# Kernel tuning notes

Measured on AMD Instinct MI355X. Metric: run time of the kernel, lower is better.

The kernel has to match this reference:

```python
import math
import jax, jax.numpy as jnp
import numpy as np

D_MODEL = 1024
H_HEADS = 16
D_K = D_MODEL // H_HEADS


def setup_inputs() -> dict:
    key = jax.random.key(0)
    ks = jax.random.split(key, 7)
    B, L = 4, 2048
    q = jax.random.normal(ks[0], (B, L, D_MODEL), dtype=jnp.float32)
    k = jax.random.normal(ks[1], (B, L, D_MODEL), dtype=jnp.float32)
    v = jax.random.normal(ks[2], (B, L, D_MODEL), dtype=jnp.float32)
    mask = jnp.ones((1, L, L), dtype=jnp.int32)
    # nn.Linear(d_model, d_model, bias=False) weights, shape (out, in)
    s = 1.0 / math.sqrt(D_MODEL)
    W_q = jax.random.uniform(ks[3], (D_MODEL, D_MODEL), jnp.float32, -s, s)
    W_k = jax.random.uniform(ks[4], (D_MODEL, D_MODEL), jnp.float32, -s, s)
    W_v = jax.random.uniform(ks[5], (D_MODEL, D_MODEL), jnp.float32, -s, s)
    W_o = jax.random.uniform(ks[6], (D_MODEL, D_MODEL), jnp.float32, -s, s)
    return {"q": q, "k": k, "v": v, "mask": mask,
            "W_q": W_q, "W_k": W_k, "W_v": W_v, "W_o": W_o}


def reference(q, k, v, mask, W_q, W_k, W_v, W_o):
    B, Lq, _ = q.shape
    # projections (Linear: x @ W.T) then split heads -> (B, H, L, d_k)
    def split_heads(x):
        return x.reshape(B, -1, H_HEADS, D_K).transpose(0, 2, 1, 3)
    Q = split_heads(jnp.einsum('bsd,ed->bse', q, W_q))
    K = split_heads(jnp.einsum('bsd,ed->bse', k, W_k))
    V = split_heads(jnp.einsum('bsd,ed->bse', v, W_v))
    # scores: (B, H, Lq, Lk)
    scores = jnp.einsum('bhqd,bhkd->bhqk', Q, K) / math.sqrt(D_K)
    m = mask[:, None, :, :]  # (1, 1, Lq, Lk) broadcast
    scores = jnp.where(m == 0, -jnp.inf, scores)
    weights = jax.nn.softmax(scores, axis=-1)
    attn = jnp.einsum('bhqk,bhkd->bhqd', weights, V)  # (B, H, Lq, d_v)
    attn = attn.transpose(0, 2, 1, 3).reshape(B, Lq, D_MODEL)
    return jnp.einsum('bse,de->bsd', attn, W_o)
```

## Files before the change

### kernel.cpp

```cpp
#include <hip/hip_runtime.h>
#include <hip/hip_bf16.h>


typedef unsigned short u16;
typedef float f32x4  __attribute__((ext_vector_type(4)));
typedef float f32x16 __attribute__((ext_vector_type(16)));
typedef short s16x8  __attribute__((ext_vector_type(8)));
typedef unsigned u32x4 __attribute__((ext_vector_type(4)));
typedef __bf16 bf16x8 __attribute__((ext_vector_type(8)));

#define QSCL 0.18033688011112042f

__device__ __forceinline__ u16 f2b(float f) {
    union { float f; unsigned u; } x; x.f = f;
    unsigned r = x.u + 0x7fffu + ((x.u >> 16) & 1u);
    return (u16)(r >> 16);
}

__device__ __forceinline__ f32x4 MF(s16x8 a, s16x8 b, f32x4 c) {
    return __builtin_amdgcn_mfma_f32_16x16x32_bf16(
        __builtin_bit_cast(bf16x8, a), __builtin_bit_cast(bf16x8, b), c, 0, 0, 0);
}
__device__ __forceinline__ f32x16 MF32(s16x8 a, s16x8 b, f32x16 c) {
    return __builtin_amdgcn_mfma_f32_32x32x16_bf16(
        __builtin_bit_cast(bf16x8, a), __builtin_bit_cast(bf16x8, b), c, 0, 0, 0);
}
__device__ __forceinline__ unsigned cvtpk(float lo, float hi) {
    unsigned r;
    asm("v_cvt_pk_bf16_f32 %0, %1, %2" : "=v"(r) : "v"(lo), "v"(hi));
    return r;
}
__device__ __forceinline__ void swap32(unsigned &a, unsigned &b) {
    asm volatile("v_permlane32_swap_b32 %0, %1" : "+v"(a), "+v"(b));
}
__device__ __forceinline__ float expa(float x) {
    float r;
    asm("v_exp_f32 %0, %1" : "=v"(r) : "v"(x));
    return r;
}
__device__ __forceinline__ void g2l16(const u16* g, u16* lbase) {
    __builtin_amdgcn_global_load_lds((const __attribute__((address_space(1))) void*)g,
                                     (__attribute__((address_space(3))) void*)lbase, 16, 0, 0);
}

__global__ __launch_bounds__(256)
void convert_and_mask(const float* __restrict__ q, const float* __restrict__ k,
                      const float* __restrict__ v, const float* __restrict__ Wq,
                      const float* __restrict__ Wk, const float* __restrict__ Wv,
                      const float* __restrict__ Wo, const int* __restrict__ mask,
                      u16* __restrict__ Abf, u16* __restrict__ Wbf,
                      int* __restrict__ mflag) {
    if (blockIdx.x < 256) {
        __shared__ int anyz;
        if (threadIdx.x == 0) anyz = 0;
        __syncthreads();
        const int qt = blockIdx.x >> 4, kt = blockIdx.x & 15;
        int local = 0;
#pragma unroll
        for (int qq = 0; qq < 16; ++qq) {
            int e4 = qq * 256 + threadIdx.x;
            int r = e4 >> 5, cc = (e4 & 31) * 4;
            int4 mv = *(const int4*)(mask + (size_t)(qt * 128 + r) * 2048 + kt * 128 + cc);
            local |= (mv.x == 0) | (mv.y == 0) | (mv.z == 0) | (mv.w == 0);
        }
        if (local) atomicOr(&anyz, 1);
        __syncthreads();
        if (threadIdx.x == 0) mflag[blockIdx.x] = anyz;
        return;
    }
    const size_t NQKV = 25165824;
    const size_t NCH  = 3670016;
    const size_t nconv = (size_t)(gridDim.x - 256) * 256;
    for (size_t cidx = (size_t)(blockIdx.x - 256) * 256 + threadIdx.x; cidx < NCH;
         cidx += nconv) {
        size_t e = cidx * 8;
        const float* src; u16* dst; float scl = 1.f;
        if (e < NQKV) {
            src = (e < 8388608) ? q + e
                : (e < 16777216) ? k + (e - 8388608) : v + (e - 16777216);
            dst = Abf + e;
        } else {
            size_t o = e - NQKV;
            if (o < 1048576)      { src = Wq + o; scl = QSCL; }
            else if (o < 2097152) { src = Wk + (o - 1048576); }
            else if (o < 3145728) { src = Wv + (o - 2097152); }
            else                  { src = Wo + (o - 3145728); }
            dst = Wbf + o;
        }
        float4 a = *(const float4*)(src);
        float4 b = *(const float4*)(src + 4);
        ushort4 p0, p1;
        p0.x = f2b(a.x * scl); p0.y = f2b(a.y * scl);
        p0.z = f2b(a.z * scl); p0.w = f2b(a.w * scl);
        p1.x = f2b(b.x * scl); p1.y = f2b(b.y * scl);
        p1.z = f2b(b.z * scl); p1.w = f2b(b.w * scl);
        *(ushort4*)dst = p0; *(ushort4*)(dst + 4) = p1;
    }
}

__global__ __launch_bounds__(256)
void gemm_qkv_fast(const u16* __restrict__ Abf, const u16* __restrict__ Wbf,
                   u16* __restrict__ Qh, u16* __restrict__ Kf, u16* __restrict__ Vf) {
    __shared__ __align__(16) u16 As[128 * 32];
    __shared__ __align__(16) u16 Bs[128 * 32];
    const int z = blockIdx.z;
    const u16* A = Abf + (size_t)z * (8192 * 1024);
    const u16* W = Wbf + (size_t)z * (1024 * 1024);
    const int tid = threadIdx.x, l = tid & 63, w = tid >> 6;
    const int g = l >> 4, c = l & 15;
    const int m0 = blockIdx.x * 128, n0 = blockIdx.y * 128;
    const int wr = (w >> 1) * 64, wc = (w & 1) * 64;

    f32x4 acc[4][4];
#pragma unroll
    for (int i = 0; i < 4; ++i)
#pragma unroll
        for (int j = 0; j < 4; ++j)
#pragma unroll
            for (int e = 0; e < 4; ++e) acc[i][j][e] = 0.f;

    const u16* Ag = A + (size_t)(m0 + w * 32 + (l >> 2)) * 1024 + (l & 3) * 8;
    const u16* Wg = W + (size_t)(n0 + w * 32 + (l >> 2)) * 1024 + (l & 3) * 8;
    u16* Al = As + w * 1024;
    u16* Bl = Bs + w * 1024;

    for (int kt = 0; kt < 32; ++kt) {
        __syncthreads();
        g2l16(Ag + kt * 32,         Al);
        g2l16(Ag + kt * 32 + 16384, Al + 512);
        g2l16(Wg + kt * 32,         Bl);
        g2l16(Wg + kt * 32 + 16384, Bl + 512);
        __syncthreads();
        s16x8 af[4], bf[4];
#pragma unroll
        for (int i = 0; i < 4; ++i) {
            af[i] = *(const s16x8*)(As + (wr + i * 16 + c) * 32 + g * 8);
            bf[i] = *(const s16x8*)(Bs + (wc + i * 16 + c) * 32 + g * 8);
        }
#pragma unroll
        for (int mi = 0; mi < 4; ++mi)
#pragma unroll
            for (int ni = 0; ni < 4; ++ni)
                acc[mi][ni] = MF(af[mi], bf[ni], acc[mi][ni]);
    }

    if (z == 0) {
#pragma unroll
        for (int mi = 0; mi < 4; ++mi)
#pragma unroll
            for (int ni = 0; ni < 4; ++ni)
#pragma unroll
                for (int j = 0; j < 4; ++j) {
                    int row = m0 + wr + mi * 16 + g * 4 + j;
                    int col = n0 + wc + ni * 16 + c;
                    int b = row >> 11, sl = row & 2047;
                    int h = col >> 6, d = col & 63;
                    Qh[(((size_t)(b * 16 + h)) * 2048 + sl) * 64 + d] = f2b(acc[mi][ni][j]);
                }
    } else if (z == 1) {
#pragma unroll
        for (int mi = 0; mi < 4; ++mi)
#pragma unroll
            for (int ni = 0; ni < 4; ++ni)
#pragma unroll
                for (int j = 0; j < 4; ++j) {
                    int row = m0 + wr + mi * 16 + g * 4 + j;
                    int col = n0 + wc + ni * 16 + c;
                    int b = row >> 11, kk = row & 2047;
                    int h = col >> 6, d = col & 63;
                    size_t off = (size_t)(b * 16 + h) * 131072
                               + (size_t)(((kk >> 5) * 4 + (d >> 4))) * 512
                               + ((kk & 31) + 32 * ((d >> 3) & 1)) * 8 + (d & 7);
                    Kf[off] = f2b(acc[mi][ni][j]);
                }
    } else {
#pragma unroll
        for (int mi = 0; mi < 4; ++mi)
#pragma unroll
            for (int ni = 0; ni < 4; ++ni) {
                int key0 = m0 + wr + mi * 16 + g * 4;
                int col  = n0 + wc + ni * 16 + c;
                int b = key0 >> 11, kk0 = key0 & 2047;
                int h = col >> 6, d = col & 63;
                size_t off = (size_t)(b * 16 + h) * 131072
                           + (size_t)((kk0 >> 6) * 8 + (d >> 5) * 4 + ((kk0 >> 4) & 3)) * 512
                           + (((kk0 >> 3) & 1) * 32 + (d & 31)) * 8 + (kk0 & 7);
                ushort4 pk;
                pk.x = f2b(acc[mi][ni][0]); pk.y = f2b(acc[mi][ni][1]);
                pk.z = f2b(acc[mi][ni][2]); pk.w = f2b(acc[mi][ni][3]);
                *(ushort4*)(Vf + off) = pk;
            }
    }
}

__global__ __launch_bounds__(256)
void gemm_out_fast(const u16* __restrict__ Ab, const u16* __restrict__ W,
                   float* __restrict__ Cout) {
    __shared__ __align__(16) u16 As[128 * 32];
    __shared__ __align__(16) u16 Bs[128 * 32];
    const int tid = threadIdx.x, l = tid & 63, w = tid >> 6;
    const int g = l >> 4, c = l & 15;
    const int m0 = blockIdx.x * 128, n0 = blockIdx.y * 128;
    const int wr = (w >> 1) * 64, wc = (w & 1) * 64;

    f32x4 acc[4][4];
#pragma unroll
    for (int i = 0; i < 4; ++i)
#pragma unroll
        for (int j = 0; j < 4; ++j)
#pragma unroll
            for (int e = 0; e < 4; ++e) acc[i][j][e] = 0.f;

    const u16* Ag = Ab + (size_t)(m0 + w * 32 + (l >> 2)) * 1024 + (l & 3) * 8;
    const u16* Wg = W  + (size_t)(n0 + w * 32 + (l >> 2)) * 1024 + (l & 3) * 8;
    u16* Al = As + w * 1024;
    u16* Bl = Bs + w * 1024;

    for (int kt = 0; kt < 32; ++kt) {
        __syncthreads();
        g2l16(Ag + kt * 32,         Al);
        g2l16(Ag + kt * 32 + 16384, Al + 512);
        g2l16(Wg + kt * 32,         Bl);
        g2l16(Wg + kt * 32 + 16384, Bl + 512);
        __syncthreads();
        s16x8 af[4], bf[4];
#pragma unroll
        for (int i = 0; i < 4; ++i) {
            af[i] = *(const s16x8*)(As + (wr + i * 16 + c) * 32 + g * 8);
            bf[i] = *(const s16x8*)(Bs + (wc + i * 16 + c) * 32 + g * 8);
        }
#pragma unroll
        for (int mi = 0; mi < 4; ++mi)
#pragma unroll
            for (int ni = 0; ni < 4; ++ni)
                acc[mi][ni] = MF(af[mi], bf[ni], acc[mi][ni]);
    }

#pragma unroll
    for (int mi = 0; mi < 4; ++mi)
#pragma unroll
        for (int ni = 0; ni < 4; ++ni)
#pragma unroll
            for (int j = 0; j < 4; ++j) {
                int row = m0 + wr + mi * 16 + g * 4 + j;
                int col = n0 + wc + ni * 16 + c;
                Cout[(size_t)row * 1024 + col] = acc[mi][ni][j];
            }
}

__global__ __launch_bounds__(256, 4)
void flash_attn(const u16* __restrict__ Qh, const u16* __restrict__ Kf,
                const u16* __restrict__ Vf, const int* __restrict__ mask,
                const int* __restrict__ mflag, u16* __restrict__ attnB) {
    __shared__ __align__(16) u16 KV[2][2][8][512];

    const int tid = threadIdx.x, w = tid >> 6, l = tid & 63;
    const int hi = l >> 5, q32 = l & 31;
    const int bh = blockIdx.x, qt = blockIdx.y;
    const size_t base = (size_t)bh * (2048 * 64);
    const u16* Qp = Qh + base;
    const u16* Kp = Kf + base;
    const u16* Vp = Vf + base;
    const int qrow_w = qt * 128 + w * 32;

    int anyflag = 0;
#pragma unroll
    for (int i = 0; i < 16; ++i) anyflag |= mflag[qt * 16 + i];

    s16x8 Qf[4];
#pragma unroll
    for (int s = 0; s < 4; ++s)
        Qf[s] = *(const s16x8*)(Qp + (size_t)(qrow_w + q32) * 64 + s * 16 + hi * 8);

    s16x8 ones;
#pragma unroll
    for (int i = 0; i < 8; ++i) ones[i] = (short)0x3F80;

    f32x16 z16;
#pragma unroll
    for (int r = 0; r < 16; ++r) z16[r] = 0.f;
    f32x16 oA = z16, oB = z16, lacc = z16;

    auto stage = [&](int buf, int kt) {
        const u16* ks = Kp + (size_t)(kt * 8 + w * 2) * 512 + l * 8;
        const u16* vs = Vp + (size_t)(kt * 8 + w * 2) * 512 + l * 8;
        g2l16(ks,       &KV[buf][0][w * 2][0]);
        g2l16(ks + 512, &KV[buf][0][w * 2 + 1][0]);
        g2l16(vs,       &KV[buf][1][w * 2][0]);
        g2l16(vs + 512, &KV[buf][1][w * 2 + 1][0]);
    };
    stage(0, 0);

    for (int kt = 0; kt < 32; ++kt) {
        const int cur = kt & 1;
        __syncthreads();
        if (kt < 31) stage(cur ^ 1, kt + 1);

        const int kr0 = kt * 64;
        const bool dom = anyflag && (mflag[qt * 16 + (kt >> 1)] != 0);

#pragma unroll
        for (int half = 0; half < 2; ++half) {
            __builtin_amdgcn_s_setprio(1);
            f32x16 s;
            {
                s16x8 ka = *(const s16x8*)&KV[cur][0][half * 4][l * 8];
                s = MF32(ka, Qf[0], z16);
            }
#pragma unroll
            for (int ss = 1; ss < 4; ++ss) {
                s16x8 ka = *(const s16x8*)&KV[cur][0][half * 4 + ss][l * 8];
                s = MF32(ka, Qf[ss], s);
            }
            __builtin_amdgcn_s_setprio(0);

            if (dom) {
                const int qr = qrow_w + q32, kb = kr0 + half * 32;
#pragma unroll
                for (int r = 0; r < 16; ++r) {
                    int key = (r & 3) + 8 * (r >> 2) + 4 * hi;
                    if (mask[(size_t)qr * 2048 + kb + key] == 0) s[r] = -1e30f;
                }
            }

#pragma unroll
            for (int r = 0; r < 16; ++r) s[r] = expa(s[r]);

            s16x8 Xp0, Xp1;
            {
                u32x4 t;
                unsigned a0 = cvtpk(s[0], s[1]),   a1 = cvtpk(s[2], s[3]);
                unsigned b0 = cvtpk(s[4], s[5]),   b1 = cvtpk(s[6], s[7]);
                swap32(a0, b0); swap32(a1, b1);
                t.x = a0; t.y = a1; t.z = b0; t.w = b1;
                Xp0 = __builtin_bit_cast(s16x8, t);
                unsigned c0 = cvtpk(s[8], s[9]),   c1 = cvtpk(s[10], s[11]);
                unsigned d0 = cvtpk(s[12], s[13]), d1 = cvtpk(s[14], s[15]);
                swap32(c0, d0); swap32(c1, d1);
                t.x = c0; t.y = c1; t.z = d0; t.w = d1;
                Xp1 = __builtin_bit_cast(s16x8, t);
            }

            __builtin_amdgcn_s_setprio(1);
            {
                s16x8 v0 = *(const s16x8*)&KV[cur][1][half * 2][l * 8];
                s16x8 v1 = *(const s16x8*)&KV[cur][1][4 + half * 2][l * 8];
                oA = MF32(Xp0, v0, oA);
                oB = MF32(Xp0, v1, oB);
                lacc = MF32(Xp0, ones, lacc);
                s16x8 v2 = *(const s16x8*)&KV[cur][1][half * 2 + 1][l * 8];
                s16x8 v3 = *(const s16x8*)&KV[cur][1][4 + half * 2 + 1][l * 8];
                oA = MF32(Xp1, v2, oA);
                oB = MF32(Xp1, v3, oB);
                lacc = MF32(Xp1, ones, lacc);
            }
            __builtin_amdgcn_s_setprio(0);
        }
    }

    const int b = bh >> 4, h = bh & 15;
#pragma unroll
    for (int r = 0; r < 16; ++r) {
        int qloc = (r & 3) + 8 * (r >> 2) + 4 * hi;
        float inv = __builtin_amdgcn_rcpf(lacc[r]);
        int row = qrow_w + qloc;
        u16* dst = attnB + ((size_t)b * 2048 + row) * 1024 + h * 64 + q32;
        dst[0]  = f2b(oA[r] * inv);
        dst[32] = f2b(oB[r] * inv);
    }
}

extern "C" void kernel_launch(void* const* d_in, const int* in_sizes, int n_in,
                              void* d_out, int out_size, void* d_ws, size_t ws_size,
                              hipStream_t stream) {
    const float* q    = (const float*)d_in[0];
    const float* k    = (const float*)d_in[1];
    const float* v    = (const float*)d_in[2];
    const int*   mask = (const int*)d_in[3];
    const float* Wq   = (const float*)d_in[4];
    const float* Wk   = (const float*)d_in[5];
    const float* Wv   = (const float*)d_in[6];
    const float* Wo   = (const float*)d_in[7];

    char* ws = (char*)d_ws;
    u16* Abf   = (u16*)(ws);
    u16* Wbf   = (u16*)(ws + (48u << 20));
    u16* Qh    = (u16*)(ws + (56u << 20));
    u16* Kf    = (u16*)(ws + (72u << 20));
    u16* Vf    = (u16*)(ws + (88u << 20));
    u16* attnB = (u16*)(ws);
    int* mflag = (int*)(ws + (104u << 20));

    convert_and_mask<<<dim3(2304), dim3(256), 0, stream>>>(q, k, v, Wq, Wk, Wv, Wo,
                                                           mask, Abf, Wbf, mflag);
    gemm_qkv_fast<<<dim3(64, 8, 3), dim3(256), 0, stream>>>(Abf, Wbf, Qh, Kf, Vf);
    flash_attn<<<dim3(64, 16), dim3(256), 0, stream>>>(Qh, Kf, Vf, mask, mflag, attnB);
    gemm_out_fast<<<dim3(64, 8), dim3(256), 0, stream>>>(attnB, Wbf + 3145728, (float*)d_out);
}
```

Before: 211.0 us.

## Software-pipeline attention loop so QK^T MFMAs overlap softmax exp of previous half

Restructures the flash-attention inner loop into a software pipeline. The second half's P·V product is deferred into the next iteration, and the S computation for the second half is issued before the exp/pack of the first half, so MFMA work can overlap the VALU exponentials. The aim is to hide exp and conversion latency behind matrix instructions. In exchange it raises register pressure, since more live f32x16 tiles are held at once, and it changes the ordering around the LDS double-buffer barrier.

```diff
diff --git a/kernel.cpp b/kernel.cpp
--- a/kernel.cpp
+++ b/kernel.cpp
@@ -289,74 +289,90 @@
         g2l16(vs,       &KV[buf][1][w * 2][0]);
         g2l16(vs + 512, &KV[buf][1][w * 2 + 1][0]);
     };
+
+    auto Shalf = [&](int buf, int half) -> f32x16 {
+        __builtin_amdgcn_s_setprio(1);
+        s16x8 ka = *(const s16x8*)&KV[buf][0][half * 4][l * 8];
+        f32x16 s = MF32(ka, Qf[0], z16);
+#pragma unroll
+        for (int ss = 1; ss < 4; ++ss) {
+            ka = *(const s16x8*)&KV[buf][0][half * 4 + ss][l * 8];
+            s = MF32(ka, Qf[ss], s);
+        }
+        __builtin_amdgcn_s_setprio(0);
+        return s;
+    };
+    auto expmask = [&](f32x16& s, int kt, int half) {
+        if (anyflag && mflag[qt * 16 + (kt >> 1)] != 0) {
+            const int qr = qrow_w + q32, kb = kt * 64 + half * 32;
+#pragma unroll
+            for (int r = 0; r < 16; ++r) {
+                int key = (r & 3) + 8 * (r >> 2) + 4 * hi;
+                if (mask[(size_t)qr * 2048 + kb + key] == 0) s[r] = -1e30f;
+            }
+        }
+#pragma unroll
+        for (int r = 0; r < 16; ++r) s[r] = expa(s[r]);
+    };
+    auto packh = [&](const f32x16& s, s16x8& X0, s16x8& X1) {
+        u32x4 t;
+        unsigned a0 = cvtpk(s[0], s[1]),   a1 = cvtpk(s[2], s[3]);
+        unsigned b0 = cvtpk(s[4], s[5]),   b1 = cvtpk(s[6], s[7]);
+        swap32(a0, b0); swap32(a1, b1);
+        t.x = a0; t.y = a1; t.z = b0; t.w = b1;
+        X0 = __builtin_bit_cast(s16x8, t);
+        unsigned c0 = cvtpk(s[8], s[9]),   c1 = cvtpk(s[10], s[11]);
+        unsigned d0 = cvtpk(s[12], s[13]), d1 = cvtpk(s[14], s[15]);
+        swap32(c0, d0); swap32(c1, d1);
+        t.x = c0; t.y = c1; t.z = d0; t.w = d1;
+        X1 = __builtin_bit_cast(s16x8, t);
+    };
+    auto PVhalf = [&](int buf, int half, s16x8 X0, s16x8 X1) {
+        __builtin_amdgcn_s_setprio(1);
+        s16x8 v0 = *(const s16x8*)&KV[buf][1][half * 2][l * 8];
+        s16x8 v1 = *(const s16x8*)&KV[buf][1][4 + half * 2][l * 8];
+        oA = MF32(X0, v0, oA);
+        oB = MF32(X0, v1, oB);
+        lacc = MF32(X0, ones, lacc);
+        s16x8 v2 = *(const s16x8*)&KV[buf][1][half * 2 + 1][l * 8];
+        s16x8 v3 = *(const s16x8*)&KV[buf][1][4 + half * 2 + 1][l * 8];
+        oA = MF32(X1, v2, oA);
+        oB = MF32(X1, v3, oB);
+        lacc = MF32(X1, ones, lacc);
+        __builtin_amdgcn_s_setprio(0);
+    };
+
+    s16x8 Xc0, Xc1;
+
     stage(0, 0);
-
-    for (int kt = 0; kt < 32; ++kt) {
-        const int cur = kt & 1;
-        __syncthreads();
-        if (kt < 31) stage(cur ^ 1, kt + 1);
-
-        const int kr0 = kt * 64;
-        const bool dom = anyflag && (mflag[qt * 16 + (kt >> 1)] != 0);
-
-#pragma unroll
-        for (int half = 0; half < 2; ++half) {
-            __builtin_amdgcn_s_setprio(1);
-            f32x16 s;
-            {
-                s16x8 ka = *(const s16x8*)&KV[cur][0][half * 4][l * 8];
-                s = MF32(ka, Qf[0], z16);
-            }
-#pragma unroll
-            for (int ss = 1; ss < 4; ++ss) {
-                s16x8 ka = *(const s16x8*)&KV[cur][0][half * 4 + ss][l * 8];
-                s = MF32(ka, Qf[ss], s);
-            }
-            __builtin_amdgcn_s_setprio(0);
-
-            if (dom) {
-                const int qr = qrow_w + q32, kb = kr0 + half * 32;
-#pragma unroll
-                for (int r = 0; r < 16; ++r) {
-                    int key = (r & 3) + 8 * (r >> 2) + 4 * hi;
-                    if (mask[(size_t)qr * 2048 + kb + key] == 0) s[r] = -1e30f;
-                }
-            }
-
-#pragma unroll
-            for (int r = 0; r < 16; ++r) s[r] = expa(s[r]);
-
-            s16x8 Xp0, Xp1;
-            {
-                u32x4 t;
-                unsigned a0 = cvtpk(s[0], s[1]),   a1 = cvtpk(s[2], s[3]);
-                unsigned b0 = cvtpk(s[4], s[5]),   b1 = cvtpk(s[6], s[7]);
-                swap32(a0, b0); swap32(a1, b1);
-                t.x = a0; t.y = a1; t.z = b0; t.w = b1;
-                Xp0 = __builtin_bit_cast(s16x8, t);
-                unsigned c0 = cvtpk(s[8], s[9]),   c1 = cvtpk(s[10], s[11]);
-                unsigned d0 = cvtpk(s[12], s[13]), d1 = cvtpk(s[14], s[15]);
-                swap32(c0, d0); swap32(c1, d1);
-                t.x = c0; t.y = c1; t.z = d0; t.w = d1;
-                Xp1 = __builtin_bit_cast(s16x8, t);
-            }
-
-            __builtin_amdgcn_s_setprio(1);
-            {
-                s16x8 v0 = *(const s16x8*)&KV[cur][1][half * 2][l * 8];
-                s16x8 v1 = *(const s16x8*)&KV[cur][1][4 + half * 2][l * 8];
-                oA = MF32(Xp0, v0, oA);
-                oB = MF32(Xp0, v1, oB);
-                lacc = MF32(Xp0, ones, lacc);
-                s16x8 v2 = *(const s16x8*)&KV[cur][1][half * 2 + 1][l * 8];
-                s16x8 v3 = *(const s16x8*)&KV[cur][1][4 + half * 2 + 1][l * 8];
-                oA = MF32(Xp1, v2, oA);
-                oB = MF32(Xp1, v3, oB);
-                lacc = MF32(Xp1, ones, lacc);
-            }
-            __builtin_amdgcn_s_setprio(0);
-        }
-    }
+    __syncthreads();
+    stage(1, 1);
+    {
+        f32x16 s0 = Shalf(0, 0);
+        expmask(s0, 0, 0);
+        f32x16 s1 = Shalf(0, 1);
+        s16x8 Y0, Y1;
+        packh(s0, Y0, Y1);
+        PVhalf(0, 0, Y0, Y1);
+        expmask(s1, 0, 1);
+        packh(s1, Xc0, Xc1);
+    }
+
+    for (int kt = 1; kt < 32; ++kt) {
+        const int buf = kt & 1, bprev = buf ^ 1;
+        PVhalf(bprev, 1, Xc0, Xc1);
+        __syncthreads();
+        if (kt < 31) stage(bprev, kt + 1);
+        f32x16 s0 = Shalf(buf, 0);
+        expmask(s0, kt, 0);
+        f32x16 s1 = Shalf(buf, 1);
+        s16x8 Y0, Y1;
+        packh(s0, Y0, Y1);
+        PVhalf(buf, 0, Y0, Y1);
+        expmask(s1, kt, 1);
+        packh(s1, Xc0, Xc1);
+    }
+    PVhalf(1, 1, Xc0, Xc1);
 
     const int b = bh >> 4, h = bh & 15;
 #pragma unroll
```

Measured after the change: 209.7 us. No clear change (-0.6%).
